# Kernel optimization log

Measured on AMD Instinct MI355X. Metric: run time of the kernel, lower is better.

## Reference

```python
import jax, jax.numpy as jnp
import numpy as np

B, L, U, H = 16, 1024, 512, 2  # batch, seq_len, units, highway_num


def setup_inputs() -> dict:
    key = jax.random.key(0)
    ks = jax.random.split(key, 8)
    s = 0.02  # weight init scale
    return {
        "inputs": jax.random.normal(ks[0], (B, L, U), dtype=jnp.float32),
        "tW": jax.random.normal(ks[1], (H, U, U), dtype=jnp.float32) * s,
        "tb": jnp.zeros((H, U), dtype=jnp.float32),
        "cW": jax.random.normal(ks[2], (H, U, U), dtype=jnp.float32) * s,
        "cb": jnp.zeros((H, U), dtype=jnp.float32),
        "aW": jax.random.normal(ks[3], (3 * U,), dtype=jnp.float32) * s,
        "ab": jnp.zeros((1,), dtype=jnp.float32),
        "frW": jax.random.normal(ks[4], (2 * U, U), dtype=jnp.float32) * s,
        "frb": jnp.zeros((U,), dtype=jnp.float32),
        "ffW": jax.random.normal(ks[5], (2 * U, U), dtype=jnp.float32) * s,
        "ffb": jnp.zeros((U,), dtype=jnp.float32),
    }


def reference(inputs, tW, tb, cW, cb, aW, ab, frW, frb, ffW, ffb):
    # Highway stack (inference: dropout is identity)
    x = inputs
    for i in range(tW.shape[0]):
        t = jax.nn.relu(x @ tW[i] + tb[i])
        c = jax.nn.sigmoid(x @ cW[i] + cb[i])
        x = t * c + x * (1.0 - c)

    # Pairwise MLP self-attention.
    # Original: A_ij = relu(dense1(concat([x_i, x_j, x_i*x_j]))).
    # Split aW = [w1; w2; w3] so we never materialize the [B,L,L,3U] tensor:
    # A_ij = relu(x_i.w1 + x_j.w2 + sum_d x_i_d * x_j_d * w3_d + b)
    u = x.shape[-1]
    w1, w2, w3 = aW[:u], aW[u:2 * u], aW[2 * u:]
    s1 = x @ w1                                    # [B,L]
    s2 = x @ w2                                    # [B,L]
    s3 = jnp.einsum('bid,bjd->bij', x * w3, x)     # [B,L,L]
    A = jax.nn.relu(s1[:, :, None] + s2[:, None, :] + s3 + ab[0])
    att = jnp.einsum('bij,bjd->bid', jax.nn.softmax(A, axis=-1), x)

    # Fuse gate. NOTE: original code uses fuse_f_dense (sigmoid) for BOTH
    # z and f (fuse_z_dense is never called), so z == f at inference.
    concat = jnp.concatenate([inputs, att], axis=-1)  # [B,L,2U]
    z = jax.nn.sigmoid(concat @ ffW + ffb)
    r = jax.nn.sigmoid(concat @ frW + frb)
    f = z
    return r * inputs + f * z
```

## Files before the change

### kernel.cpp

```cpp
#include <hip/hip_runtime.h>
#include <math.h>

typedef __bf16 bf16;
typedef __attribute__((ext_vector_type(8))) __bf16 bf16x8;
typedef __attribute__((ext_vector_type(4))) float f32x4;

#define CDIV(a,b) (((a)+(b)-1)/(b))


__device__ __forceinline__ void load_lds16(const bf16* g, bf16* l) {
  __builtin_amdgcn_global_load_lds(
      (const __attribute__((address_space(1))) unsigned int*)(g),
      (__attribute__((address_space(3))) unsigned int*)(l), 16, 0, 0);
}

struct GemmArgs {
  const bf16* A; const bf16* B; bf16* C;
  int K, lda, ldb, ldc;
  long long Ab, Bb, Cb;
  const float* s1; const float* s2; const float* abp;
  int L;
  int gxsh, gysh;
};

template<int EPI>
__global__ __launch_bounds__(256, 4)
void gemm_nt(GemmArgs g) {
  __shared__ bf16 As[128 * 64];
  __shared__ bf16 Bs[128 * 64];
  const int tid = threadIdx.x;
  const int bid = blockIdx.x;
  const int xcd = bid & 7;
  const int t = bid >> 3;
  const int bx = t & ((1 << g.gxsh) - 1);
  const int r  = t >> g.gxsh;
  const int Rx = gridDim.x >> (3 + g.gxsh);
  const int gr = xcd * Rx + r;
  const int by = gr & ((1 << g.gysh) - 1);
  const int bz = gr >> g.gysh;

  const bf16* Ag = g.A + (long long)bz * g.Ab + (long long)(by * 128) * g.lda;
  const bf16* Bg = g.B + (long long)bz * g.Bb + (long long)(bx * 128) * g.ldb;
  const int wid = tid >> 6, lane = tid & 63;
  const int wm = (wid >> 1) << 6;
  const int wn = (wid & 1) << 6;
  const int lr = lane & 15, lq = lane >> 4;

  f32x4 acc[4][4];
#pragma unroll
  for (int i = 0; i < 4; i++)
#pragma unroll
    for (int j = 0; j < 4; j++) acc[i][j] = f32x4{0.f, 0.f, 0.f, 0.f};

  const int srow8 = (tid >> 3) & 7;
  const int skc   = (tid & 7) ^ srow8;
  const int lswz  = (lr & 7);

  for (int k0 = 0; k0 < g.K; k0 += 64) {
    __syncthreads();
#pragma unroll
    for (int j = 0; j < 4; j++) {
      const int ci = (tid >> 6) * 4 + j;
      const int row = ci * 8 + srow8;
      load_lds16(Ag + (long long)row * g.lda + k0 + skc * 8, As + ci * 512);
      load_lds16(Bg + (long long)row * g.ldb + k0 + skc * 8, Bs + ci * 512);
    }
    __syncthreads();
#pragma unroll
    for (int ks = 0; ks < 2; ks++) {
      bf16x8 af[4], bfr[4];
      const int kx = (ks * 4 + lq) ^ lswz;
#pragma unroll
      for (int i = 0; i < 4; i++)
        af[i] = *(const bf16x8*)(&As[(wm + i * 16 + lr) * 64 + kx * 8]);
#pragma unroll
      for (int j = 0; j < 4; j++)
        bfr[j] = *(const bf16x8*)(&Bs[(wn + j * 16 + lr) * 64 + kx * 8]);
#pragma unroll
      for (int i = 0; i < 4; i++)
#pragma unroll
        for (int j = 0; j < 4; j++)
          acc[i][j] = __builtin_amdgcn_mfma_f32_16x16x32_bf16(af[i], bfr[j], acc[i][j], 0, 0, 0);
    }
  }

  bf16* Cg = g.C + (long long)bz * g.Cb;
#pragma unroll
  for (int i = 0; i < 4; i++) {
#pragma unroll
    for (int v = 0; v < 4; v++) {
      int row = by * 128 + wm + i * 16 + lq * 4 + v;
      float srow = 0.f;
      if (EPI == 1) srow = g.s1[bz * g.L + row] + g.abp[0];
#pragma unroll
      for (int j = 0; j < 4; j++) {
        int col = bx * 128 + wn + j * 16 + lr;
        float val = acc[i][j][v];
        if (EPI == 1) { val += srow + g.s2[bz * g.L + col]; val = fmaxf(val, 0.f); }
        Cg[(long long)row * g.ldc + col] = (bf16)val;
      }
    }
  }
}

struct DualArgs {
  const bf16* A; const bf16* A2;
  const bf16* Bt;
  void* C; const void* xres;
  const float* bias_t; const float* bias_c;
  int K, ldb;
};

template<int EPI>
__global__ __launch_bounds__(256, 4)
void gemm_dual(DualArgs g) {
  __shared__ bf16 As[128 * 64];
  __shared__ bf16 Bs[128 * 64];
  const int tid = threadIdx.x;
  const int bid = blockIdx.x;
  const int xcd = bid & 7;
  const int t = bid >> 3;
  const int bx = t & 7;
  const int r  = t >> 3;
  const int Rx = gridDim.x >> 6;
  const int by = xcd * Rx + r;

  const int wid = tid >> 6, lane = tid & 63;
  const int wm = (wid >> 1) << 6;
  const int wn = (wid & 1) << 6;
  const int lr = lane & 15, lq = lane >> 4;

  f32x4 acc[4][4];
#pragma unroll
  for (int i = 0; i < 4; i++)
#pragma unroll
    for (int j = 0; j < 4; j++) acc[i][j] = f32x4{0.f, 0.f, 0.f, 0.f};

  const int srow8 = (tid >> 3) & 7;
  const int skc   = (tid & 7) ^ srow8;
  const int lswz  = (lr & 7);
  const long long abase = (long long)(by * 128) * 512;

  for (int k0 = 0; k0 < g.K; k0 += 64) {
    const bf16* Ak = (k0 < 512) ? g.A : g.A2;
    const int kk = k0 & 511;
    __syncthreads();
#pragma unroll
    for (int j = 0; j < 4; j++) {
      const int ci = (tid >> 6) * 4 + j;
      const int bn = ci * 8 + srow8;
      load_lds16(Ak + abase + (long long)bn * 512 + kk + skc * 8, As + ci * 512);
      const int grp = bn >> 5, r5 = bn & 31;
      const int grow = ((grp & 1) << 9) + bx * 64 + ((grp >> 1) << 5) + r5;
      load_lds16(g.Bt + (long long)grow * g.ldb + k0 + skc * 8, Bs + ci * 512);
    }
    __syncthreads();
#pragma unroll
    for (int ks = 0; ks < 2; ks++) {
      bf16x8 af[4], bfr[4];
      const int kx = (ks * 4 + lq) ^ lswz;
#pragma unroll
      for (int i = 0; i < 4; i++)
        af[i] = *(const bf16x8*)(&As[(wm + i * 16 + lr) * 64 + kx * 8]);
#pragma unroll
      for (int j = 0; j < 4; j++)
        bfr[j] = *(const bf16x8*)(&Bs[(wn + j * 16 + lr) * 64 + kx * 8]);
#pragma unroll
      for (int i = 0; i < 4; i++)
#pragma unroll
        for (int j = 0; j < 4; j++)
          acc[i][j] = __builtin_amdgcn_mfma_f32_16x16x32_bf16(af[i], bfr[j], acc[i][j], 0, 0, 0);
    }
  }

  const int colb = bx * 64 + (wn >> 1);
#pragma unroll
  for (int i = 0; i < 4; i++) {
#pragma unroll
    for (int v = 0; v < 4; v++) {
      int row = by * 128 + wm + i * 16 + lq * 4 + v;
#pragma unroll
      for (int j = 0; j < 2; j++) {
        int col = colb + j * 16 + lr;
        long long idx = (long long)row * 512 + col;
        float p0 = acc[i][j][v] + g.bias_t[col];
        float p1 = acc[i][j + 2][v] + g.bias_c[col];
        if (EPI == 0) {
          float tt = fmaxf(p0, 0.f);
          float c = 1.f / (1.f + __expf(-p1));
          float x = (float)((const bf16*)g.xres)[idx];
          ((bf16*)g.C)[idx] = (bf16)(tt * c + x * (1.f - c));
        } else {
          float z = 1.f / (1.f + __expf(-p0));
          float rr = 1.f / (1.f + __expf(-p1));
          float x = ((const float*)g.xres)[idx];
          ((float*)g.C)[idx] = rr * x + z * z;
        }
      }
    }
  }
}

__global__ void wprep(const float* tW, const float* tb, const float* cW, const float* cb,
                      const float* frW, const float* frb, const float* ffW, const float* ffb,
                      bf16* w1T, bf16* w2T, float* bias1, float* bias2) {
  int idx = blockIdx.x * 256 + threadIdx.x;
  const int N1 = 1048576, N2 = 1048576;
  if (idx < N1) {
    int l = idx >> 19;
    int rem = idx & 524287;
    int n = rem >> 9, k = rem & 511;
    float v = (n < 512) ? tW[l * 262144 + k * 512 + n]
                        : cW[l * 262144 + k * 512 + (n - 512)];
    w1T[idx] = (bf16)v;
  } else if (idx < N1 + N2) {
    int j = idx - N1;
    int n = j >> 10, k = j & 1023;
    float v = (n < 512) ? ffW[k * 512 + n] : frW[k * 512 + (n - 512)];
    w2T[j] = (bf16)v;
  } else if (idx < N1 + N2 + 3072) {
    int j = idx - (N1 + N2);
    if (j < 2048) {
      int l = j >> 10, n = j & 1023;
      bias1[j] = (n < 512) ? tb[l * 512 + n] : cb[l * 512 + (n - 512)];
    } else {
      int n = j - 2048;
      bias2[n] = (n < 512) ? ffb[n] : frb[n - 512];
    }
  }
}

__global__ void init_conv(const float* inp, bf16* xb0) {
  long long i8 = ((long long)blockIdx.x * 256 + threadIdx.x) * 8;
  bf16x8 o;
#pragma unroll
  for (int k = 0; k < 8; k++) o[k] = (bf16)inp[i8 + k];
  *(bf16x8*)(xb0 + i8) = o;
}

__global__ void s1s2q_k(const bf16* x, const float* aW, float* s1, float* s2, bf16* q16) {
  int wid = threadIdx.x >> 6, lane = threadIdx.x & 63;
  int m = blockIdx.x * 4 + wid;
  long long base = (long long)m * 512;
  int d0 = lane * 8;
  bf16x8 xv = *(const bf16x8*)(x + base + d0);
  float a1 = 0.f, a2 = 0.f;
  bf16x8 o;
#pragma unroll
  for (int k = 0; k < 8; k++) {
    float xx = (float)xv[k];
    a1 += xx * aW[d0 + k];
    a2 += xx * aW[512 + d0 + k];
    o[k] = (bf16)(xx * aW[1024 + d0 + k]);
  }
  *(bf16x8*)(q16 + base + d0) = o;
  for (int off = 32; off; off >>= 1) {
    a1 += __shfl_down(a1, off, 64);
    a2 += __shfl_down(a2, off, 64);
  }
  if (!lane) { s1[m] = a1; s2[m] = a2; }
}

__global__ __launch_bounds__(256) void transpose_k(const bf16* xb, bf16* xT) {
  __shared__ bf16 t[64][65];
  int b = blockIdx.z;
  int d0 = blockIdx.x * 64, j0 = blockIdx.y * 64;
  const bf16* src = xb + (long long)b * 524288;
  bf16* dst = xT + (long long)b * 524288;
  int tid = threadIdx.x;
  int rr = tid >> 3, cc = (tid & 7) * 8;
#pragma unroll
  for (int it = 0; it < 2; ++it) {
    int r = rr + it * 32;
    bf16x8 v = *(const bf16x8*)(src + (long long)(j0 + r) * 512 + d0 + cc);
#pragma unroll
    for (int k = 0; k < 8; k++) t[cc + k][r] = v[k];
  }
  __syncthreads();
#pragma unroll
  for (int it = 0; it < 2; ++it) {
    int r = rr + it * 32;
    bf16x8 v;
#pragma unroll
    for (int k = 0; k < 8; k++) v[k] = t[r][cc + k];
    *(bf16x8*)(dst + (long long)(d0 + r) * 1024 + j0 + cc) = v;
  }
}

__global__ __launch_bounds__(256) void softmax_k(bf16* S) {
  __shared__ float red[8];
  long long base = (long long)blockIdx.x * 1024;
  int tid = threadIdx.x, lane = tid & 63, wid = tid >> 6;
  float v[4];
#pragma unroll
  for (int i = 0; i < 4; i++) v[i] = (float)S[base + tid + 256 * i];
  float m = fmaxf(fmaxf(v[0], v[1]), fmaxf(v[2], v[3]));
  for (int off = 32; off; off >>= 1) m = fmaxf(m, __shfl_down(m, off, 64));
  if (!lane) red[wid] = m;
  __syncthreads();
  m = fmaxf(fmaxf(red[0], red[1]), fmaxf(red[2], red[3]));
  float e[4], s = 0.f;
#pragma unroll
  for (int i = 0; i < 4; i++) { e[i] = __expf(v[i] - m); s += e[i]; }
  for (int off = 32; off; off >>= 1) s += __shfl_down(s, off, 64);
  if (!lane) red[4 + wid] = s;
  __syncthreads();
  float inv = 1.f / (red[4] + red[5] + red[6] + red[7]);
#pragma unroll
  for (int i = 0; i < 4; i++) S[base + tid + 256 * i] = (bf16)(e[i] * inv);
}

extern "C" void kernel_launch(void* const* d_in, const int* in_sizes, int n_in,
                              void* d_out, int out_size, void* d_ws, size_t ws_size,
                              hipStream_t stream) {
  const float* inp = (const float*)d_in[0];
  const float* tW  = (const float*)d_in[1];
  const float* tb  = (const float*)d_in[2];
  const float* cW  = (const float*)d_in[3];
  const float* cb  = (const float*)d_in[4];
  const float* aW  = (const float*)d_in[5];
  const float* ab  = (const float*)d_in[6];
  const float* frW = (const float*)d_in[7];
  const float* frb = (const float*)d_in[8];
  const float* ffW = (const float*)d_in[9];
  const float* ffb = (const float*)d_in[10];
  float* out = (float*)d_out;

  char* p = (char*)d_ws;
  auto alloc = [&](size_t bytes) { char* r = p; p += (bytes + 255) & ~size_t(255); return r; };
  bf16* xb0   = (bf16*) alloc(16777216);
  bf16* x1    = (bf16*) alloc(16777216);
  bf16* x2    = (bf16*) alloc(16777216);
  bf16* q16   = (bf16*) alloc(16777216);
  bf16* xT16  = (bf16*) alloc(16777216);
  bf16* att16 = (bf16*) alloc(16777216);
  bf16* preS  = (bf16*) alloc(33554432);
  float* s1   = (float*)alloc(65536);
  float* s2   = (float*)alloc(65536);
  bf16* w1T   = (bf16*) alloc(2097152);
  bf16* w2T   = (bf16*) alloc(2097152);
  float* bias1= (float*)alloc(8192);
  float* bias2= (float*)alloc(4096);

  wprep<<<CDIV(1048576 + 1048576 + 3072, 256), 256, 0, stream>>>(
      tW, tb, cW, cb, frW, frb, ffW, ffb, w1T, w2T, bias1, bias2);
  init_conv<<<4096, 256, 0, stream>>>(inp, xb0);

  {
    const bf16* xin[2] = {xb0, x1};
    bf16* xout[2] = {x1, x2};
    for (int l = 0; l < 2; l++) {
      DualArgs g{};
      g.A = xin[l]; g.A2 = xin[l]; g.Bt = w1T + (long long)l * 524288;
      g.C = xout[l]; g.xres = xin[l];
      g.bias_t = bias1 + l * 1024; g.bias_c = bias1 + l * 1024 + 512;
      g.K = 512; g.ldb = 512;
      gemm_dual<0><<<1024, 256, 0, stream>>>(g);
    }
  }

  s1s2q_k<<<4096, 256, 0, stream>>>(x2, aW, s1, s2, q16);
  transpose_k<<<dim3(8, 16, 16), 256, 0, stream>>>(x2, xT16);

  {
    GemmArgs g{};
    g.A = q16; g.B = x2; g.C = preS;
    g.K = 512; g.lda = 512; g.ldb = 512; g.ldc = 1024;
    g.Ab = 524288; g.Bb = 524288; g.Cb = 1048576;
    g.s1 = s1; g.s2 = s2; g.abp = ab; g.L = 1024;
    g.gxsh = 3; g.gysh = 3;
    gemm_nt<1><<<1024, 256, 0, stream>>>(g);
  }
  softmax_k<<<16384, 256, 0, stream>>>(preS);
  {
    GemmArgs g{};
    g.A = preS; g.B = xT16; g.C = att16;
    g.K = 1024; g.lda = 1024; g.ldb = 1024; g.ldc = 512;
    g.Ab = 1048576; g.Bb = 524288; g.Cb = 524288;
    g.gxsh = 2; g.gysh = 3;
    gemm_nt<2><<<512, 256, 0, stream>>>(g);
  }
  {
    DualArgs g{};
    g.A = xb0; g.A2 = att16; g.Bt = w2T;
    g.C = out; g.xres = inp;
    g.bias_t = bias2; g.bias_c = bias2 + 512;
    g.K = 1024; g.ldb = 1024;
    gemm_dual<1><<<1024, 256, 0, stream>>>(g);
  }
}
```

Before: 291.1 us.

## Fuse softmax into attention GEMMs and s1/s2/q into highway epilogue

Drops the standalone softmax kernel. The score GEMM epilogue now writes exp(relu(score)) clamped at 60 with no max subtraction, which is valid because relu bounds the values below. It also atomically accumulates the row sums, and the PV GEMM scales each output row by the reciprocal row sum. It also drops the s1s2q kernel by computing the s1/s2 dot products and the q tensor in the second highway GEMM's epilogue using shuffles and atomics. This removes two full passes over large intermediates, at the cost of atomic contention, an extra memset, and softmax numerics that deviate only if scores exceed the clamp.

```diff
diff --git a/kernel.cpp b/kernel.cpp
--- a/kernel.cpp
+++ b/kernel.cpp
@@ -19,6 +19,7 @@
   int K, lda, ldb, ldc;
   long long Ab, Bb, Cb;
   const float* s1; const float* s2; const float* abp;
+  float* lsum;
   int L;
   int gxsh, gysh;
 };
@@ -92,12 +93,30 @@
       int row = by * 128 + wm + i * 16 + lq * 4 + v;
       float srow = 0.f;
       if (EPI == 1) srow = g.s1[bz * g.L + row] + g.abp[0];
+      if (EPI == 4) srow = 1.f / g.s1[bz * g.L + row];
+      float psum = 0.f;
 #pragma unroll
       for (int j = 0; j < 4; j++) {
         int col = bx * 128 + wn + j * 16 + lr;
         float val = acc[i][j][v];
-        if (EPI == 1) { val += srow + g.s2[bz * g.L + col]; val = fmaxf(val, 0.f); }
-        Cg[(long long)row * g.ldc + col] = (bf16)val;
+        if (EPI == 1) {
+          val += srow + g.s2[bz * g.L + col];
+          val = fminf(fmaxf(val, 0.f), 60.f);
+          val = __expf(val);
+          bf16 eb = (bf16)val;
+          psum += (float)eb;
+          Cg[(long long)row * g.ldc + col] = eb;
+        } else {
+          val *= srow;
+          Cg[(long long)row * g.ldc + col] = (bf16)val;
+        }
+      }
+      if (EPI == 1) {
+        psum += __shfl_xor(psum, 1, 64);
+        psum += __shfl_xor(psum, 2, 64);
+        psum += __shfl_xor(psum, 4, 64);
+        psum += __shfl_xor(psum, 8, 64);
+        if (lr == 0) atomicAdd(&g.lsum[bz * g.L + row], psum);
       }
     }
   }
@@ -109,6 +128,9 @@
   void* C; const void* xres;
   const float* bias_t; const float* bias_c;
   int K, ldb;
+  const float* aW;
+  float* s1a; float* s2a;
+  bf16* q;
 };
 
 template<int EPI>
@@ -179,22 +201,44 @@
 #pragma unroll
     for (int v = 0; v < 4; v++) {
       int row = by * 128 + wm + i * 16 + lq * 4 + v;
+      float p1s = 0.f, p2s = 0.f;
 #pragma unroll
       for (int j = 0; j < 2; j++) {
         int col = colb + j * 16 + lr;
         long long idx = (long long)row * 512 + col;
         float p0 = acc[i][j][v] + g.bias_t[col];
         float p1 = acc[i][j + 2][v] + g.bias_c[col];
-        if (EPI == 0) {
-          float tt = fmaxf(p0, 0.f);
-          float c = 1.f / (1.f + __expf(-p1));
-          float x = (float)((const bf16*)g.xres)[idx];
-          ((bf16*)g.C)[idx] = (bf16)(tt * c + x * (1.f - c));
-        } else {
+        if (EPI == 1) {
           float z = 1.f / (1.f + __expf(-p0));
           float rr = 1.f / (1.f + __expf(-p1));
           float x = ((const float*)g.xres)[idx];
           ((float*)g.C)[idx] = rr * x + z * z;
+        } else {
+          float tt = fmaxf(p0, 0.f);
+          float c = 1.f / (1.f + __expf(-p1));
+          float x = (float)((const bf16*)g.xres)[idx];
+          bf16 xn = (bf16)(tt * c + x * (1.f - c));
+          ((bf16*)g.C)[idx] = xn;
+          if (EPI == 2) {
+            float xf = (float)xn;
+            p1s += xf * g.aW[col];
+            p2s += xf * g.aW[512 + col];
+            g.q[idx] = (bf16)(xf * g.aW[1024 + col]);
+          }
+        }
+      }
+      if (EPI == 2) {
+        p1s += __shfl_xor(p1s, 1, 64);
+        p1s += __shfl_xor(p1s, 2, 64);
+        p1s += __shfl_xor(p1s, 4, 64);
+        p1s += __shfl_xor(p1s, 8, 64);
+        p2s += __shfl_xor(p2s, 1, 64);
+        p2s += __shfl_xor(p2s, 2, 64);
+        p2s += __shfl_xor(p2s, 4, 64);
+        p2s += __shfl_xor(p2s, 8, 64);
+        if (lr == 0) {
+          atomicAdd(&g.s1a[row], p1s);
+          atomicAdd(&g.s2a[row], p2s);
         }
       }
     }
@@ -238,29 +282,6 @@
   *(bf16x8*)(xb0 + i8) = o;
 }
 
-__global__ void s1s2q_k(const bf16* x, const float* aW, float* s1, float* s2, bf16* q16) {
-  int wid = threadIdx.x >> 6, lane = threadIdx.x & 63;
-  int m = blockIdx.x * 4 + wid;
-  long long base = (long long)m * 512;
-  int d0 = lane * 8;
-  bf16x8 xv = *(const bf16x8*)(x + base + d0);
-  float a1 = 0.f, a2 = 0.f;
-  bf16x8 o;
-#pragma unroll
-  for (int k = 0; k < 8; k++) {
-    float xx = (float)xv[k];
-    a1 += xx * aW[d0 + k];
-    a2 += xx * aW[512 + d0 + k];
-    o[k] = (bf16)(xx * aW[1024 + d0 + k]);
-  }
-  *(bf16x8*)(q16 + base + d0) = o;
-  for (int off = 32; off; off >>= 1) {
-    a1 += __shfl_down(a1, off, 64);
-    a2 += __shfl_down(a2, off, 64);
-  }
-  if (!lane) { s1[m] = a1; s2[m] = a2; }
-}
-
 __global__ __launch_bounds__(256) void transpose_k(const bf16* xb, bf16* xT) {
   __shared__ bf16 t[64][65];
   int b = blockIdx.z;
@@ -285,29 +306,6 @@
     for (int k = 0; k < 8; k++) v[k] = t[r][cc + k];
     *(bf16x8*)(dst + (long long)(d0 + r) * 1024 + j0 + cc) = v;
   }
-}
-
-__global__ __launch_bounds__(256) void softmax_k(bf16* S) {
-  __shared__ float red[8];
-  long long base = (long long)blockIdx.x * 1024;
-  int tid = threadIdx.x, lane = tid & 63, wid = tid >> 6;
-  float v[4];
-#pragma unroll
-  for (int i = 0; i < 4; i++) v[i] = (float)S[base + tid + 256 * i];
-  float m = fmaxf(fmaxf(v[0], v[1]), fmaxf(v[2], v[3]));
-  for (int off = 32; off; off >>= 1) m = fmaxf(m, __shfl_down(m, off, 64));
-  if (!lane) red[wid] = m;
-  __syncthreads();
-  m = fmaxf(fmaxf(red[0], red[1]), fmaxf(red[2], red[3]));
-  float e[4], s = 0.f;
-#pragma unroll
-  for (int i = 0; i < 4; i++) { e[i] = __expf(v[i] - m); s += e[i]; }
-  for (int off = 32; off; off >>= 1) s += __shfl_down(s, off, 64);
-  if (!lane) red[4 + wid] = s;
-  __syncthreads();
-  float inv = 1.f / (red[4] + red[5] + red[6] + red[7]);
-#pragma unroll
-  for (int i = 0; i < 4; i++) S[base + tid + 256 * i] = (bf16)(e[i] * inv);
 }
 
 extern "C" void kernel_launch(void* const* d_in, const int* in_sizes, int n_in,
@@ -334,51 +332,56 @@
   bf16* q16   = (bf16*) alloc(16777216);
   bf16* xT16  = (bf16*) alloc(16777216);
   bf16* att16 = (bf16*) alloc(16777216);
-  bf16* preS  = (bf16*) alloc(33554432);
-  float* s1   = (float*)alloc(65536);
-  float* s2   = (float*)alloc(65536);
+  bf16* E16   = (bf16*) alloc(33554432);
+  float* sred = (float*)alloc(196608);
   bf16* w1T   = (bf16*) alloc(2097152);
   bf16* w2T   = (bf16*) alloc(2097152);
   float* bias1= (float*)alloc(8192);
   float* bias2= (float*)alloc(4096);
-
+  float* s1 = sred, *s2 = sred + 16384, *lsum = sred + 32768;
+
+  hipMemsetAsync(sred, 0, 196608, stream);
   wprep<<<CDIV(1048576 + 1048576 + 3072, 256), 256, 0, stream>>>(
       tW, tb, cW, cb, frW, frb, ffW, ffb, w1T, w2T, bias1, bias2);
   init_conv<<<4096, 256, 0, stream>>>(inp, xb0);
 
   {
-    const bf16* xin[2] = {xb0, x1};
-    bf16* xout[2] = {x1, x2};
-    for (int l = 0; l < 2; l++) {
-      DualArgs g{};
-      g.A = xin[l]; g.A2 = xin[l]; g.Bt = w1T + (long long)l * 524288;
-      g.C = xout[l]; g.xres = xin[l];
-      g.bias_t = bias1 + l * 1024; g.bias_c = bias1 + l * 1024 + 512;
-      g.K = 512; g.ldb = 512;
-      gemm_dual<0><<<1024, 256, 0, stream>>>(g);
-    }
-  }
-
-  s1s2q_k<<<4096, 256, 0, stream>>>(x2, aW, s1, s2, q16);
+    DualArgs g{};
+    g.A = xb0; g.A2 = xb0; g.Bt = w1T;
+    g.C = x1; g.xres = xb0;
+    g.bias_t = bias1; g.bias_c = bias1 + 512;
+    g.K = 512; g.ldb = 512;
+    gemm_dual<0><<<1024, 256, 0, stream>>>(g);
+  }
+  {
+    DualArgs g{};
+    g.A = x1; g.A2 = x1; g.Bt = w1T + 524288;
+    g.C = x2; g.xres = x1;
+    g.bias_t = bias1 + 1024; g.bias_c = bias1 + 1536;
+    g.K = 512; g.ldb = 512;
+    g.aW = aW; g.s1a = s1; g.s2a = s2; g.q = q16;
+    gemm_dual<2><<<1024, 256, 0, stream>>>(g);
+  }
+
   transpose_k<<<dim3(8, 16, 16), 256, 0, stream>>>(x2, xT16);
 
   {
     GemmArgs g{};
-    g.A = q16; g.B = x2; g.C = preS;
+    g.A = q16; g.B = x2; g.C = E16;
     g.K = 512; g.lda = 512; g.ldb = 512; g.ldc = 1024;
     g.Ab = 524288; g.Bb = 524288; g.Cb = 1048576;
-    g.s1 = s1; g.s2 = s2; g.abp = ab; g.L = 1024;
+    g.s1 = s1; g.s2 = s2; g.abp = ab; g.lsum = lsum; g.L = 1024;
     g.gxsh = 3; g.gysh = 3;
     gemm_nt<1><<<1024, 256, 0, stream>>>(g);
   }
-  softmax_k<<<16384, 256, 0, stream>>>(preS);
   {
     GemmArgs g{};
-    g.A = preS; g.B = xT16; g.C = att16;
+    g.A = E16; g.B = xT16; g.C = att16;
     g.K = 1024; g.lda = 1024; g.ldb = 1024; g.ldc = 512;
     g.Ab = 1048576; g.Bb = 524288; g.Cb = 524288;
+    g.s1 = lsum; g.L = 1024;
     g.gxsh = 2; g.gysh = 3;
-    gemm_nt<2><<<512, 256, 0, stream>>>(g);
+    gemm_nt<4><<<512, 256, 0, stream>>>(g);
   }
   {
     DualArgs g{};
```

New measurement: 271.7 us. -6.6%, faster.
